# Performance work log

Hardware: AMD Instinct MI355X
Metric: run time of the kernel (lower is better)

Reference implementation:

```python
import jax, jax.numpy as jnp
import numpy as np

GDEP = 2
ALPHA = 0.05

def setup_inputs() -> dict:
    key = jax.random.key(0)
    ks = jax.random.split(key, 6)
    B, C, V, L = 8, 32, 512, 256  # L = c_in * num_patterns
    x = jax.random.normal(ks[0], (B, C, V, L), dtype=jnp.float32)
    adj = jax.random.uniform(ks[1], (B, V, V), dtype=jnp.float32)
    W = jax.random.normal(ks[2], (L, L), dtype=jnp.float32) * (1.0 / np.sqrt(L))
    b = jax.random.normal(ks[3], (L,), dtype=jnp.float32) * (1.0 / np.sqrt(L))
    conv_w = jax.random.normal(ks[4], (C, (GDEP + 1) * C, 1, 1), dtype=jnp.float32) * 0.1
    conv_b = jax.random.normal(ks[5], (C,), dtype=jnp.float32) * 0.1
    return {"x": x, "adj": adj, "W": W, "b": b, "conv_w": conv_w, "conv_b": conv_b}

def reference(x, adj, W, b, conv_w, conv_b):
    B, C, V, L = x.shape
    # adj normalization: add self loops, divide by column-sums (sum over dim 1)
    adj_new = adj + jnp.eye(V, dtype=adj.dtype)[None]          # [B,V,V]
    d = adj_new.sum(axis=1)[:, None, :]                        # [B,1,V]
    a = adj_new / d                                            # [B,V,V]
    h = x
    out = [h]
    for _ in range(GDEP):
        hw = h @ W + b                                         # [B,C,V,L] (matmul on last dim)
        diff = jnp.einsum('ncwl,nvw->ncvl', hw, a)             # hypergraph diffusion over nodes
        h = ALPHA * x + (1.0 - ALPHA) * diff
        out.append(h)
    ho = jnp.concatenate(out, axis=1)                          # [B,(gdep+1)*C,V,L]
    # 1x1 Conv2d == channel-mixing einsum
    w2 = conv_w[:, :, 0, 0]                                    # [C_out, (gdep+1)*C]
    ho = jnp.einsum('bcvl,oc->bovl', ho, w2) + conv_b[None, :, None, None]
    return ho
```

## Files before the change

### kernel.cpp

```cpp
#include <hip/hip_runtime.h>

constexpr int NB = 8;
constexpr int NC = 32;
constexpr int NV = 512;
constexpr int NL = 256;
constexpr float F_ALPHA = 0.05f;
constexpr float F_BETA  = 0.95f;

typedef __bf16 bf16x8 __attribute__((ext_vector_type(8)));
typedef float  f32x4  __attribute__((ext_vector_type(4)));

__device__ __forceinline__ void async_ld16(const void* g, void* l) {
  __builtin_amdgcn_global_load_lds(
      (const __attribute__((address_space(1))) void*)g,
      (__attribute__((address_space(3))) void*)l, 16, 0, 0);
}


__global__ void k_colsum_part(const float* __restrict__ adj, float* __restrict__ partial) {
  int idx = blockIdx.x * 256 + threadIdx.x;
  int w = idx & 511;
  int chunk = (idx >> 9) & 7;
  int n = idx >> 12;
  const float* p = adj + n * (NV * NV) + chunk * 64 * NV + w;
  float s = 0.f;
#pragma unroll
  for (int v = 0; v < 64; ++v) s += p[v * NV];
  partial[idx] = s;
}

__global__ void k_dinv(const float* __restrict__ partial, float* __restrict__ dinv) {
  int idx = blockIdx.x * 256 + threadIdx.x;
  int w = idx & 511;
  int n = idx >> 9;
  float s = 1.f;
#pragma unroll
  for (int j = 0; j < 8; ++j) s += partial[n * 4096 + j * 512 + w];
  dinv[idx] = 1.f / s;
}

__global__ void k_prep_a(const float* __restrict__ adj, const float* __restrict__ dinv,
                         __bf16* __restrict__ a) {
  int idx = blockIdx.x * 256 + threadIdx.x;
  int w = idx & 511;
  int v = (idx >> 9) & 511;
  int n = idx >> 18;
  float val = adj[idx] + (v == w ? 1.0f : 0.0f);
  a[idx] = (__bf16)(val * dinv[(n << 9) | w]);
}

__global__ void k_prep_wt(const float* __restrict__ W, __bf16* __restrict__ Wt) {
  int idx = blockIdx.x * 256 + threadIdx.x;
  int l = idx >> 8, k = idx & 255;
  Wt[idx] = (__bf16)W[(k << 8) | l];
}

template <bool BF32>
__global__ __launch_bounds__(256, 2)
void k_gemm_wt(const __bf16* __restrict__ Wt, const void* __restrict__ Bsrc,
               const float* __restrict__ bias, __bf16* __restrict__ hw) {
  __shared__ __align__(16) char lds[32768];
  char* ldsA = lds;
  char* ldsB = lds + 16384;

  const int tid = threadIdx.x;
  const int bid = blockIdx.x;
  const int p = bid >> 3;
  const int mtile = (bid >> 2) & 1;
  const int ntile = bid & 3;
  const int n = p >> 5, c = p & 31;

  int Bbase, Bstride;
  if (BF32) { Bbase = p * (NV * NL); Bstride = NL; }
  else      { Bbase = n * (NV * NC * NL) + c * NL; Bstride = NC * NL; }

  const int wave = tid >> 6, lane = tid & 63;
  const int quad = lane >> 4, l16 = lane & 15;
  const int wm = wave >> 1, wn = wave & 1;
  const int wbase = (tid & ~63) * 16;

  f32x4 acc[4][4];
#pragma unroll
  for (int i = 0; i < 4; ++i)
#pragma unroll
    for (int j = 0; j < 4; ++j) acc[i][j] = (f32x4){0.f, 0.f, 0.f, 0.f};

  for (int kt = 0; kt < 256 / 64; ++kt) {
    __syncthreads();
#pragma unroll
    for (int j = 0; j < 4; ++j) {
      int pos = j * 4096 + tid * 16;
      int row = pos >> 7;
      int kb = (pos & 127) ^ ((row & 7) * 16);
      const __bf16* g = Wt + (mtile * 128 + row) * 256 + kt * 64 + (kb >> 1);
      async_ld16(g, ldsA + j * 4096 + wbase);
    }
    if (BF32) {
      const float* Bf = (const float*)Bsrc;
#pragma unroll
      for (int j = 0; j < 4; ++j) {
        int pos = j * 4096 + tid * 16;
        int row = pos >> 7;
        int kb = (pos & 127) ^ ((row & 7) * 16);
        const float* g = Bf + Bbase + (ntile * 128 + row) * Bstride + kt * 64 + (kb >> 1);
        float4 f0 = *(const float4*)g;
        float4 f1 = *(const float4*)(g + 4);
        bf16x8 vv;
        vv[0] = (__bf16)f0.x; vv[1] = (__bf16)f0.y; vv[2] = (__bf16)f0.z; vv[3] = (__bf16)f0.w;
        vv[4] = (__bf16)f1.x; vv[5] = (__bf16)f1.y; vv[6] = (__bf16)f1.z; vv[7] = (__bf16)f1.w;
        *(bf16x8*)(ldsB + pos) = vv;
      }
    } else {
      const __bf16* Bf = (const __bf16*)Bsrc;
#pragma unroll
      for (int j = 0; j < 4; ++j) {
        int pos = j * 4096 + tid * 16;
        int row = pos >> 7;
        int kb = (pos & 127) ^ ((row & 7) * 16);
        const __bf16* g = Bf + Bbase + (ntile * 128 + row) * Bstride + kt * 64 + (kb >> 1);
        async_ld16(g, ldsB + j * 4096 + wbase);
      }
    }
    __syncthreads();
#pragma unroll
    for (int ks = 0; ks < 2; ++ks) {
      bf16x8 af[4], bfr[4];
#pragma unroll
      for (int mb = 0; mb < 4; ++mb) {
        int m = wm * 64 + mb * 16 + l16;
        int kb = (ks * 64 + quad * 16) ^ ((m & 7) * 16);
        af[mb] = *(const bf16x8*)(ldsA + m * 128 + kb);
      }
#pragma unroll
      for (int nb = 0; nb < 4; ++nb) {
        int nn = wn * 64 + nb * 16 + l16;
        int kb = (ks * 64 + quad * 16) ^ ((nn & 7) * 16);
        bfr[nb] = *(const bf16x8*)(ldsB + nn * 128 + kb);
      }
#pragma unroll
      for (int mb = 0; mb < 4; ++mb)
#pragma unroll
        for (int nb = 0; nb < 4; ++nb)
          acc[mb][nb] = __builtin_amdgcn_mfma_f32_16x16x32_bf16(af[mb], bfr[nb], acc[mb][nb], 0, 0, 0);
    }
  }
  __bf16* outp = hw + p * (NL * NV) + mtile * 128 * NV + ntile * 128;
#pragma unroll
  for (int mb = 0; mb < 4; ++mb) {
#pragma unroll
    for (int r = 0; r < 4; ++r) {
      int ml = wm * 64 + mb * 16 + quad * 4 + r;
      float bv = bias[mtile * 128 + ml];
#pragma unroll
      for (int nb = 0; nb < 4; ++nb) {
        int nl = wn * 64 + nb * 16 + l16;
        outp[ml * NV + nl] = (__bf16)(acc[mb][nb][r] + bv);
      }
    }
  }
}

__global__ __launch_bounds__(256, 2)
void k_gemm_a(const __bf16* __restrict__ abuf, const __bf16* __restrict__ hw,
              const float* __restrict__ x, __bf16* __restrict__ hout) {
  __shared__ __align__(16) char lds[32768];
  char* ldsA = lds;
  char* ldsB = lds + 16384;

  const int tid = threadIdx.x;
  const int bid = blockIdx.x;
  const int n = bid >> 8;
  const int mtile = (bid >> 6) & 3;
  const int ntile = bid & 63;

  const __bf16* Ab = abuf + n * (NV * NV) + mtile * 128 * NV;
  const __bf16* Bb = hw + n * (NC * NL * NV) + ntile * 128 * NV;

  const int wave = tid >> 6, lane = tid & 63;
  const int quad = lane >> 4, l16 = lane & 15;
  const int wm = wave >> 1, wn = wave & 1;
  const int wbase = (tid & ~63) * 16;

  f32x4 acc[4][4];
#pragma unroll
  for (int i = 0; i < 4; ++i)
#pragma unroll
    for (int j = 0; j < 4; ++j) acc[i][j] = (f32x4){0.f, 0.f, 0.f, 0.f};

  for (int kt = 0; kt < 512 / 64; ++kt) {
    __syncthreads();
#pragma unroll
    for (int j = 0; j < 4; ++j) {
      int pos = j * 4096 + tid * 16;
      int row = pos >> 7;
      int kb = (pos & 127) ^ ((row & 7) * 16);
      async_ld16(Ab + row * NV + kt * 64 + (kb >> 1), ldsA + j * 4096 + wbase);
    }
#pragma unroll
    for (int j = 0; j < 4; ++j) {
      int pos = j * 4096 + tid * 16;
      int row = pos >> 7;
      int kb = (pos & 127) ^ ((row & 7) * 16);
      async_ld16(Bb + row * NV + kt * 64 + (kb >> 1), ldsB + j * 4096 + wbase);
    }
    __syncthreads();
#pragma unroll
    for (int ks = 0; ks < 2; ++ks) {
      bf16x8 af[4], bfr[4];
#pragma unroll
      for (int mb = 0; mb < 4; ++mb) {
        int m = wm * 64 + mb * 16 + l16;
        int kb = (ks * 64 + quad * 16) ^ ((m & 7) * 16);
        af[mb] = *(const bf16x8*)(ldsA + m * 128 + kb);
      }
#pragma unroll
      for (int nb = 0; nb < 4; ++nb) {
        int nn = wn * 64 + nb * 16 + l16;
        int kb = (ks * 64 + quad * 16) ^ ((nn & 7) * 16);
        bfr[nb] = *(const bf16x8*)(ldsB + nn * 128 + kb);
      }
#pragma unroll
      for (int mb = 0; mb < 4; ++mb)
#pragma unroll
        for (int nb = 0; nb < 4; ++nb)
          acc[mb][nb] = __builtin_amdgcn_mfma_f32_16x16x32_bf16(af[mb], bfr[nb], acc[mb][nb], 0, 0, 0);
    }
  }
#pragma unroll
  for (int mb = 0; mb < 4; ++mb) {
#pragma unroll
    for (int r = 0; r < 4; ++r) {
      int v = mtile * 128 + wm * 64 + mb * 16 + quad * 4 + r;
#pragma unroll
      for (int nb = 0; nb < 4; ++nb) {
        int col = ntile * 128 + wn * 64 + nb * 16 + l16;
        int c = col >> 8, l = col & 255;
        float xv = x[((n * NC + c) * NV + v) * NL + l];
        hout[n * (NV * NC * NL) + v * (NC * NL) + col] =
            (__bf16)(F_ALPHA * xv + F_BETA * acc[mb][nb][r]);
      }
    }
  }
}

__global__ __launch_bounds__(256, 2)
void k_conv(const float* __restrict__ x, const __bf16* __restrict__ h1,
            const __bf16* __restrict__ h2, const float* __restrict__ cw,
            const float* __restrict__ cb, float* __restrict__ out) {
  __shared__ __align__(16) char lds[288 * 208];
  char* Bt = lds;
  char* Aw = lds + 256 * 208;

  const int tid = threadIdx.x;
  const int bid = blockIdx.x;
  const int n = bid >> 9, v = bid & 511;

  for (int i = tid; i < 3072; i += 256) {
    int o = i / 96, k = i - o * 96;
    *(__bf16*)(Aw + o * 208 + k * 2) = (__bf16)cw[i];
  }

  {
    const int l = tid;
    bf16x8 pk;
    const float* xp = x + n * (NC * NV * NL) + v * NL + l;
#pragma unroll
    for (int c = 0; c < 32; ++c) {
      pk[c & 7] = (__bf16)xp[c * (NV * NL)];
      if ((c & 7) == 7) *(bf16x8*)(Bt + l * 208 + (c - 7) * 2) = pk;
    }
    const __bf16* hp1 = h1 + (n * NV + v) * (NC * NL) + l;
#pragma unroll
    for (int c = 0; c < 32; ++c) {
      pk[c & 7] = hp1[c * NL];
      if ((c & 7) == 7) *(bf16x8*)(Bt + l * 208 + (32 + c - 7) * 2) = pk;
    }
    const __bf16* hp2 = h2 + (n * NV + v) * (NC * NL) + l;
#pragma unroll
    for (int c = 0; c < 32; ++c) {
      pk[c & 7] = hp2[c * NL];
      if ((c & 7) == 7) *(bf16x8*)(Bt + l * 208 + (64 + c - 7) * 2) = pk;
    }
  }
  __syncthreads();

  const int wave = tid >> 6, lane = tid & 63;
  const int quad = lane >> 4, l16 = lane & 15;

  f32x4 acc[2][4];
#pragma unroll
  for (int i = 0; i < 2; ++i)
#pragma unroll
    for (int j = 0; j < 4; ++j) acc[i][j] = (f32x4){0.f, 0.f, 0.f, 0.f};

#pragma unroll
  for (int ks = 0; ks < 3; ++ks) {
    bf16x8 af[2], bfr[4];
#pragma unroll
    for (int mt = 0; mt < 2; ++mt) {
      int m = mt * 16 + l16;
      af[mt] = *(const bf16x8*)(Aw + m * 208 + ks * 64 + quad * 16);
    }
#pragma unroll
    for (int nb = 0; nb < 4; ++nb) {
      int ll = wave * 64 + nb * 16 + l16;
      bfr[nb] = *(const bf16x8*)(Bt + ll * 208 + ks * 64 + quad * 16);
    }
#pragma unroll
    for (int mt = 0; mt < 2; ++mt)
#pragma unroll
      for (int nb = 0; nb < 4; ++nb)
        acc[mt][nb] = __builtin_amdgcn_mfma_f32_16x16x32_bf16(af[mt], bfr[nb], acc[mt][nb], 0, 0, 0);
  }

#pragma unroll
  for (int mt = 0; mt < 2; ++mt) {
#pragma unroll
    for (int r = 0; r < 4; ++r) {
      int o = mt * 16 + quad * 4 + r;
      float bo = cb[o];
#pragma unroll
      for (int nb = 0; nb < 4; ++nb) {
        int ll = wave * 64 + nb * 16 + l16;
        out[((n * NC + o) * NV + v) * NL + ll] = acc[mt][nb][r] + bo;
      }
    }
  }
}

extern "C" void kernel_launch(void* const* d_in, const int* in_sizes, int n_in,
                              void* d_out, int out_size, void* d_ws, size_t ws_size,
                              hipStream_t stream) {
  const float* x   = (const float*)d_in[0];
  const float* adj = (const float*)d_in[1];
  const float* W   = (const float*)d_in[2];
  const float* b   = (const float*)d_in[3];
  const float* cw  = (const float*)d_in[4];
  const float* cb  = (const float*)d_in[5];
  float* out = (float*)d_out;
  char* ws = (char*)d_ws;

  float*  dinv    = (float*)ws;
  float*  partial = (float*)(ws + 16384);
  __bf16* Wt      = (__bf16*)(ws + 147456);
  __bf16* abuf    = (__bf16*)(ws + 278528);
  __bf16* hwbuf   = (__bf16*)(ws + 4472832);
  __bf16* h1      = (__bf16*)(ws + 4472832 + 67108864);
  __bf16* h2      = (__bf16*)(ws + 4472832 + 2 * 67108864);

  k_colsum_part<<<128, 256, 0, stream>>>(adj, partial);
  k_dinv<<<16, 256, 0, stream>>>(partial, dinv);
  k_prep_a<<<8192, 256, 0, stream>>>(adj, dinv, abuf);
  k_prep_wt<<<256, 256, 0, stream>>>(W, Wt);

  k_gemm_wt<true><<<2048, 256, 0, stream>>>(Wt, (const void*)x, b, hwbuf);
  k_gemm_a<<<2048, 256, 0, stream>>>(abuf, hwbuf, x, h1);
  k_gemm_wt<false><<<2048, 256, 0, stream>>>(Wt, (const void*)h1, b, hwbuf);
  k_gemm_a<<<2048, 256, 0, stream>>>(abuf, hwbuf, x, h2);

  k_conv<<<4096, 256, 0, stream>>>(x, h1, h2, cw, cb, out);
}
```

Before: 497.7 us.

## Replace MFMA conv kernel with vectorized FP32 FMA channel-mixing kernel

The 1x1 conv epilogue no longer stages x/h1/h2 into LDS as bf16 and runs MFMA. Instead each thread loads four consecutive l positions with vector loads and accumulates all 32 output channels in registers using fp32 FMAs, with weights read from LDS in fp32. This removes the LDS transpose, the scalar strided loads and the bf16 rounding of x and the weights. In exchange it does FMA work on vector ALUs instead of matrix cores and holds 128 accumulator registers per thread, which may lower occupancy.

```diff
diff --git a/kernel.cpp b/kernel.cpp
--- a/kernel.cpp
+++ b/kernel.cpp
@@ -8,6 +8,7 @@
 constexpr float F_BETA  = 0.95f;
 
 typedef __bf16 bf16x8 __attribute__((ext_vector_type(8)));
+typedef __bf16 bf16x4 __attribute__((ext_vector_type(4)));
 typedef float  f32x4  __attribute__((ext_vector_type(4)));
 
 __device__ __forceinline__ void async_ld16(const void* g, void* l) {
@@ -244,87 +245,67 @@
 }
 
 __global__ __launch_bounds__(256, 2)
-void k_conv(const float* __restrict__ x, const __bf16* __restrict__ h1,
-            const __bf16* __restrict__ h2, const float* __restrict__ cw,
-            const float* __restrict__ cb, float* __restrict__ out) {
-  __shared__ __align__(16) char lds[288 * 208];
-  char* Bt = lds;
-  char* Aw = lds + 256 * 208;
-
+void k_conv_vec(const float* __restrict__ x, const __bf16* __restrict__ h1,
+                const __bf16* __restrict__ h2, const float* __restrict__ cw,
+                const float* __restrict__ cb, float* __restrict__ out) {
+  __shared__ float w2s[32 * 96];
   const int tid = threadIdx.x;
+  for (int i = tid; i < 32 * 96; i += 256) w2s[i] = cw[i];
+  __syncthreads();
+
   const int bid = blockIdx.x;
-  const int n = bid >> 9, v = bid & 511;
-
-  for (int i = tid; i < 3072; i += 256) {
-    int o = i / 96, k = i - o * 96;
-    *(__bf16*)(Aw + o * 208 + k * 2) = (__bf16)cw[i];
-  }
-
-  {
-    const int l = tid;
-    bf16x8 pk;
-    const float* xp = x + n * (NC * NV * NL) + v * NL + l;
-#pragma unroll
-    for (int c = 0; c < 32; ++c) {
-      pk[c & 7] = (__bf16)xp[c * (NV * NL)];
-      if ((c & 7) == 7) *(bf16x8*)(Bt + l * 208 + (c - 7) * 2) = pk;
-    }
-    const __bf16* hp1 = h1 + (n * NV + v) * (NC * NL) + l;
-#pragma unroll
-    for (int c = 0; c < 32; ++c) {
-      pk[c & 7] = hp1[c * NL];
-      if ((c & 7) == 7) *(bf16x8*)(Bt + l * 208 + (32 + c - 7) * 2) = pk;
-    }
-    const __bf16* hp2 = h2 + (n * NV + v) * (NC * NL) + l;
-#pragma unroll
-    for (int c = 0; c < 32; ++c) {
-      pk[c & 7] = hp2[c * NL];
-      if ((c & 7) == 7) *(bf16x8*)(Bt + l * 208 + (64 + c - 7) * 2) = pk;
-    }
-  }
-  __syncthreads();
-
-  const int wave = tid >> 6, lane = tid & 63;
-  const int quad = lane >> 4, l16 = lane & 15;
-
-  f32x4 acc[2][4];
-#pragma unroll
-  for (int i = 0; i < 2; ++i)
-#pragma unroll
-    for (int j = 0; j < 4; ++j) acc[i][j] = (f32x4){0.f, 0.f, 0.f, 0.f};
-
-#pragma unroll
-  for (int ks = 0; ks < 3; ++ks) {
-    bf16x8 af[2], bfr[4];
-#pragma unroll
-    for (int mt = 0; mt < 2; ++mt) {
-      int m = mt * 16 + l16;
-      af[mt] = *(const bf16x8*)(Aw + m * 208 + ks * 64 + quad * 16);
-    }
-#pragma unroll
-    for (int nb = 0; nb < 4; ++nb) {
-      int ll = wave * 64 + nb * 16 + l16;
-      bfr[nb] = *(const bf16x8*)(Bt + ll * 208 + ks * 64 + quad * 16);
-    }
-#pragma unroll
-    for (int mt = 0; mt < 2; ++mt)
-#pragma unroll
-      for (int nb = 0; nb < 4; ++nb)
-        acc[mt][nb] = __builtin_amdgcn_mfma_f32_16x16x32_bf16(af[mt], bfr[nb], acc[mt][nb], 0, 0, 0);
-  }
-
-#pragma unroll
-  for (int mt = 0; mt < 2; ++mt) {
-#pragma unroll
-    for (int r = 0; r < 4; ++r) {
-      int o = mt * 16 + quad * 4 + r;
-      float bo = cb[o];
-#pragma unroll
-      for (int nb = 0; nb < 4; ++nb) {
-        int ll = wave * 64 + nb * 16 + l16;
-        out[((n * NC + o) * NV + v) * NL + ll] = acc[mt][nb][r] + bo;
-      }
-    }
+  const int n = bid >> 7;
+  const int v = ((bid & 127) << 2) + (tid >> 6);
+  const int l = (tid & 63) << 2;
+
+  const float*  px = x  + (n * NC * NV + v) * NL + l;
+  const __bf16* p1 = h1 + (n * NV + v) * (NC * NL) + l;
+  const __bf16* p2 = h2 + (n * NV + v) * (NC * NL) + l;
+
+  f32x4 acc[32];
+#pragma unroll
+  for (int o = 0; o < 32; ++o) acc[o] = (f32x4){0.f, 0.f, 0.f, 0.f};
+
+#pragma unroll
+  for (int kb = 0; kb < 12; ++kb) {
+    f32x4 val[8];
+#pragma unroll
+    for (int j = 0; j < 8; ++j) {
+      int k = kb * 8 + j;
+      if (k < 32) {
+        float4 t = *(const float4*)(px + k * (NV * NL));
+        val[j] = (f32x4){t.x, t.y, t.z, t.w};
+      } else if (k < 64) {
+        bf16x4 t = *(const bf16x4*)(p1 + (k - 32) * NL);
+        val[j] = (f32x4){(float)t[0], (float)t[1], (float)t[2], (float)t[3]};
+      } else {
+        bf16x4 t = *(const bf16x4*)(p2 + (k - 64) * NL);
+        val[j] = (f32x4){(float)t[0], (float)t[1], (float)t[2], (float)t[3]};
+      }
+    }
+#pragma unroll
+    for (int o = 0; o < 32; ++o) {
+      const float* wr = &w2s[o * 96 + kb * 8];
+      f32x4 wA = *(const f32x4*)wr;
+      f32x4 wB = *(const f32x4*)(wr + 4);
+      acc[o] += val[0] * wA[0];
+      acc[o] += val[1] * wA[1];
+      acc[o] += val[2] * wA[2];
+      acc[o] += val[3] * wA[3];
+      acc[o] += val[4] * wB[0];
+      acc[o] += val[5] * wB[1];
+      acc[o] += val[6] * wB[2];
+      acc[o] += val[7] * wB[3];
+    }
+  }
+
+  float* po = out + (n * NC * NV + v) * NL + l;
+#pragma unroll
+  for (int o = 0; o < 32; ++o) {
+    float bo = cb[o];
+    f32x4 r = acc[o];
+    float4 s = {r[0] + bo, r[1] + bo, r[2] + bo, r[3] + bo};
+    *(float4*)(po + o * (NV * NL)) = s;
   }
 }
 
@@ -358,5 +339,5 @@
   k_gemm_wt<false><<<2048, 256, 0, stream>>>(Wt, (const void*)h1, b, hwbuf);
   k_gemm_a<<<2048, 256, 0, stream>>>(abuf, hwbuf, x, h2);
 
-  k_conv<<<4096, 256, 0, stream>>>(x, h1, h2, cw, cb, out);
-}
+  k_conv_vec<<<1024, 256, 0, stream>>>(x, h1, h2, cw, cb, out);
+}
```

Measured after the change: 877.7 us. 1.76x slower.
